# Optimization experiments

Hardware: AMD Instinct MI355X
Metric: run time of the kernel (lower is better)

The kernel has to match this reference:

```python
import jax, jax.numpy as jnp
import numpy as np
import math

D = 1024
N_HEAD = 16
HEAD_D = D // N_HEAD

def setup_inputs() -> dict:
    key = jax.random.key(0)
    ks = jax.random.split(key, 10)
    b, s = 4, 2048
    scale = 1.0 / math.sqrt(D)
    inp = {
        "decoder_hs": jax.random.normal(ks[0], (b, s, D), dtype=jnp.float32),
        "encoder_hs": jax.random.normal(ks[1], (b, s, D), dtype=jnp.float32),
        "Wq": jax.random.normal(ks[2], (D, D), dtype=jnp.float32) * scale,
        "bq": jnp.zeros((D,), dtype=jnp.float32),
        "Wk": jax.random.normal(ks[3], (D, D), dtype=jnp.float32) * scale,
        "bk": jnp.zeros((D,), dtype=jnp.float32),
        "Wv": jax.random.normal(ks[4], (D, D), dtype=jnp.float32) * scale,
        "bv": jnp.zeros((D,), dtype=jnp.float32),
        "Wp": jax.random.normal(ks[5], (D, D), dtype=jnp.float32) * scale,
        "bp": jnp.zeros((D,), dtype=jnp.float32),
    }
    return inp

def _split_heads(x, b, s):
    # [b, s, d] -> [b, n_head, s, head_d]
    return x.reshape(b, s, N_HEAD, HEAD_D).transpose(0, 2, 1, 3)

def reference(decoder_hs, encoder_hs, Wq, bq, Wk, bk, Wv, bv, Wp, bp):
    b, s, d = decoder_hs.shape
    # torch nn.Linear: y = x @ W.T + b
    q = _split_heads(decoder_hs @ Wq.T + bq, b, s)
    k = _split_heads(encoder_hs @ Wk.T + bk, b, s)
    v = _split_heads(encoder_hs @ Wv.T + bv, b, s)
    att = jnp.einsum('bhqd,bhkd->bhqk', q, k) * (1.0 / math.sqrt(HEAD_D))
    att = jax.nn.softmax(att, axis=-1)  # mask is None, dropout = 0 (eval)
    y = jnp.einsum('bhqk,bhkd->bhqd', att, v)
    y = y.transpose(0, 2, 1, 3).reshape(b, s, d)
    return y @ Wp.T + bp
```

## Files before the change

kernel.cpp:

```cpp
#include <hip/hip_runtime.h>
#include <hip/hip_bf16.h>

typedef __attribute__((ext_vector_type(8))) short bf16x8;
typedef __attribute__((ext_vector_type(4))) float floatx4;

#define MFMA_16x16x32(A, B, C) __builtin_amdgcn_mfma_f32_16x16x32_bf16(A, B, C, 0, 0, 0)

__device__ __forceinline__ unsigned short f2b(float f) {
    __hip_bfloat16 h = __float2bfloat16(f);
    unsigned short u;
    __builtin_memcpy(&u, &h, 2);
    return u;
}
__device__ __forceinline__ unsigned pk2(float a, float b) {
    __hip_bfloat162 h = __float22bfloat162_rn(float2{a, b});
    unsigned u;
    __builtin_memcpy(&u, &h, 4);
    return u;
}
__device__ __forceinline__ void async_lds16(const void* g, void* l) {
    __builtin_amdgcn_global_load_lds((__attribute__((address_space(1))) void*)g,
                                     (__attribute__((address_space(3))) void*)l, 16, 0, 0);
}

struct CvtArgs {
    const float* src[6];
    unsigned short* dst[6];
    float scale[6];
    int n8[6];
};
__global__ __launch_bounds__(256) void convert_kernel(CvtArgs a) {
    const int t = blockIdx.y;
    const int i = blockIdx.x * 256 + threadIdx.x;
    if (i >= a.n8[t]) return;
    const float sc = a.scale[t];
    const float4* s = (const float4*)a.src[t];
    const float4 x = s[2 * i], y = s[2 * i + 1];
    bf16x8 v;
    v[0] = (short)f2b(x.x * sc); v[1] = (short)f2b(x.y * sc);
    v[2] = (short)f2b(x.z * sc); v[3] = (short)f2b(x.w * sc);
    v[4] = (short)f2b(y.x * sc); v[5] = (short)f2b(y.y * sc);
    v[6] = (short)f2b(y.z * sc); v[7] = (short)f2b(y.w * sc);
    *(bf16x8*)(a.dst[t] + (size_t)i * 8) = v;
}

struct QKVArgs {
    const unsigned short* A[3];
    const unsigned short* B[3];
    const float* bias[3];
    float bscale[3];
    unsigned short* C[3];
};
__global__ __launch_bounds__(256) void gemm_qkv(QKVArgs args) {
    constexpr int M = 8192, N = 1024, K = 1024;
    __shared__ __align__(16) unsigned short As[2][4096];
    __shared__ __align__(16) unsigned short Bs[2][4096];

    const int z = blockIdx.z;
    const unsigned short* __restrict__ A = args.A[z];
    const unsigned short* __restrict__ B = args.B[z];
    const float* __restrict__ bias = args.bias[z];
    const float bsc = args.bscale[z];
    unsigned short* __restrict__ C = args.C[z];

    const int tid  = threadIdx.x;
    const int wave = tid >> 6;
    const int lane = tid & 63;
    const int l16  = lane & 15;
    const int quad = lane >> 4;
    const int bm = (blockIdx.x & 63) * 128;
    const int bn = (blockIdx.x >> 6) * 128;
    const int wm = (wave >> 1) * 64;
    const int wn = (wave & 1) * 64;

    const int srow = tid >> 2;
    const int skb  = (tid & 3) * 8;

    floatx4 acc[4][4] = {};

    auto stage = [&](int buf, int k0) {
        async_lds16(A + (size_t)(bm + srow) * K + skb + k0, &As[buf][tid * 8]);
        async_lds16(A + (size_t)(bm + 64 + srow) * K + skb + k0, &As[buf][2048 + tid * 8]);
        async_lds16(B + (size_t)(bn + srow) * K + skb + k0, &Bs[buf][tid * 8]);
        async_lds16(B + (size_t)(bn + 64 + srow) * K + skb + k0, &Bs[buf][2048 + tid * 8]);
    };

    stage(0, 0);
    for (int it = 0; it < K / 32; ++it) {
        __syncthreads();
        if (it + 1 < K / 32) stage((it + 1) & 1, (it + 1) * 32);
        const unsigned short* Ac = &As[it & 1][0];
        const unsigned short* Bc = &Bs[it & 1][0];

        bf16x8 af[4], bfr[4];
        #pragma unroll
        for (int i = 0; i < 4; ++i)
            af[i] = *(const bf16x8*)&Ac[(wm + i * 16 + l16) * 32 + quad * 8];
        #pragma unroll
        for (int j = 0; j < 4; ++j)
            bfr[j] = *(const bf16x8*)&Bc[(wn + j * 16 + l16) * 32 + quad * 8];
        #pragma unroll
        for (int i = 0; i < 4; ++i)
            #pragma unroll
            for (int j = 0; j < 4; ++j)
                acc[i][j] = MFMA_16x16x32(af[i], bfr[j], acc[i][j]);
    }

    if (z == 2) {
        __syncthreads();
        unsigned short* Tw = &As[0][0] + wave * (16 * 66);
        #pragma unroll
        for (int j = 0; j < 4; ++j) {
            const float bv = bias[bn + wn + j * 16 + l16] * bsc;
            #pragma unroll
            for (int i = 0; i < 4; ++i)
                #pragma unroll
                for (int r = 0; r < 4; ++r)
                    Tw[l16 * 66 + i * 16 + quad * 4 + r] = f2b(acc[i][j][r] + bv);
            __syncthreads();
            const int c2  = lane >> 2;
            const int tch = lane & 3;
            bf16x8 t0 = *(const bf16x8*)&Tw[c2 * 66 + tch * 16];
            bf16x8 t1 = *(const bf16x8*)&Tw[c2 * 66 + tch * 16 + 8];
            const size_t off = (size_t)(bn + wn + j * 16 + c2) * (size_t)M + (bm + wm + tch * 16);
            *(bf16x8*)&C[off]     = t0;
            *(bf16x8*)&C[off + 8] = t1;
            __syncthreads();
        }
    } else {
        #pragma unroll
        for (int i = 0; i < 4; ++i) {
            const int row = bm + wm + i * 16 + quad * 4;
            #pragma unroll
            for (int j = 0; j < 4; ++j) {
                const int col = bn + wn + j * 16 + l16;
                const float bv = bias[col] * bsc;
                #pragma unroll
                for (int r = 0; r < 4; ++r)
                    C[(size_t)(row + r) * N + col] = f2b(acc[i][j][r] + bv);
            }
        }
    }
}

__global__ __launch_bounds__(256) void gemm_out(
    const unsigned short* __restrict__ A, const unsigned short* __restrict__ B,
    const float* __restrict__ bias, float* __restrict__ C,
    int M, int N, int K)
{
    __shared__ __align__(16) unsigned short As[2][4096];
    __shared__ __align__(16) unsigned short Bs[2][4096];

    const int tid  = threadIdx.x;
    const int wave = tid >> 6;
    const int lane = tid & 63;
    const int l16  = lane & 15;
    const int quad = lane >> 4;
    const int bm = (blockIdx.x & 63) * 128;
    const int bn = (blockIdx.x >> 6) * 128;
    const int wm = (wave >> 1) * 64;
    const int wn = (wave & 1) * 64;

    const int srow = tid >> 2;
    const int skb  = (tid & 3) * 8;

    floatx4 acc[4][4] = {};

    auto stage = [&](int buf, int k0) {
        async_lds16(A + (size_t)(bm + srow) * K + skb + k0, &As[buf][tid * 8]);
        async_lds16(A + (size_t)(bm + 64 + srow) * K + skb + k0, &As[buf][2048 + tid * 8]);
        async_lds16(B + (size_t)(bn + srow) * K + skb + k0, &Bs[buf][tid * 8]);
        async_lds16(B + (size_t)(bn + 64 + srow) * K + skb + k0, &Bs[buf][2048 + tid * 8]);
    };

    stage(0, 0);
    for (int it = 0; it < K / 32; ++it) {
        __syncthreads();
        if (it + 1 < K / 32) stage((it + 1) & 1, (it + 1) * 32);
        const unsigned short* Ac = &As[it & 1][0];
        const unsigned short* Bc = &Bs[it & 1][0];

        bf16x8 af[4], bfr[4];
        #pragma unroll
        for (int i = 0; i < 4; ++i)
            af[i] = *(const bf16x8*)&Ac[(wm + i * 16 + l16) * 32 + quad * 8];
        #pragma unroll
        for (int j = 0; j < 4; ++j)
            bfr[j] = *(const bf16x8*)&Bc[(wn + j * 16 + l16) * 32 + quad * 8];
        #pragma unroll
        for (int i = 0; i < 4; ++i)
            #pragma unroll
            for (int j = 0; j < 4; ++j)
                acc[i][j] = MFMA_16x16x32(af[i], bfr[j], acc[i][j]);
    }

    #pragma unroll
    for (int i = 0; i < 4; ++i) {
        const int row = bm + wm + i * 16 + quad * 4;
        #pragma unroll
        for (int j = 0; j < 4; ++j) {
            const int col = bn + wn + j * 16 + l16;
            const float bv = bias[col];
            #pragma unroll
            for (int r = 0; r < 4; ++r)
                C[(size_t)(row + r) * N + col] = acc[i][j][r] + bv;
        }
    }
}

__global__ __launch_bounds__(512, 4) void attn_kernel(
    const unsigned short* __restrict__ Q, const unsigned short* __restrict__ Kg,
    const unsigned short* __restrict__ Vt, unsigned short* __restrict__ Y)
{
    __shared__ __align__(16) unsigned short Ks[2][4096];
    __shared__ __align__(16) unsigned short Vs[2][4096];
    __shared__ __align__(16) unsigned short Pt[8][32 * 68];

    const int tid  = threadIdx.x;
    const int wave = tid >> 6;
    const int lane = tid & 63;
    const int l16  = lane & 15;
    const int quad = lane >> 4;
    const int bh = blockIdx.x & 63;
    const int qt = blockIdx.x >> 6;
    const int b  = bh >> 4;
    const int h  = bh & 15;
    const int q0 = qt * 256 + wave * 32;
    const size_t base  = ((size_t)b * 2048) * 1024 + (size_t)h * 64;
    const size_t vbase = ((size_t)h * 64) * 8192 + (size_t)b * 2048;

    bf16x8 qf[2][2];
    #pragma unroll
    for (int nt = 0; nt < 2; ++nt) {
        const size_t qoff = base + (size_t)(q0 + nt * 16 + l16) * 1024 + quad * 8;
        qf[nt][0] = *(const bf16x8*)&Q[qoff];
        qf[nt][1] = *(const bf16x8*)&Q[qoff + 32];
    }

    bf16x8 ones;
    #pragma unroll
    for (int e = 0; e < 8; ++e) ones[e] = (short)0x3F80;
    const floatx4 ZERO4 = {0.f, 0.f, 0.f, 0.f};

    floatx4 o[2][4] = {};
    floatx4 rs[2] = {};

    const int rl_ = tid >> 3;
    const int cb  = tid & 7;
    const int csw = cb ^ (rl_ & 7);
    const int swz = l16 & 7;
    const int sw0 = (quad ^ swz) * 8;
    const int sw1 = ((4 + quad) ^ swz) * 8;
    const int krow = l16 * 64;
    const int prow = l16 * 68;
    const int pcol = quad * 4;

    unsigned short* Pw = &Pt[wave][0];

    auto stage = [&](int buf, int kv0) {
        async_lds16(&Kg[base + (size_t)(kv0 + rl_) * 1024 + csw * 8], &Ks[buf][tid * 8]);
        async_lds16(&Vt[vbase + (size_t)rl_ * 8192 + kv0 + csw * 8], &Vs[buf][tid * 8]);
    };

    stage(0, 0);
    for (int t = 0; t < 32; ++t) {
        __syncthreads();
        if (t < 31) stage((t + 1) & 1, (t + 1) * 64);
        const unsigned short* Kc = &Ks[t & 1][0];
        const unsigned short* Vc = &Vs[t & 1][0];

        floatx4 st[4][2];
        #pragma unroll
        for (int mt = 0; mt < 4; ++mt) {
            const bf16x8 kf0 = *(const bf16x8*)&Kc[mt * 1024 + krow + sw0];
            const bf16x8 kf1 = *(const bf16x8*)&Kc[mt * 1024 + krow + sw1];
            #pragma unroll
            for (int nt = 0; nt < 2; ++nt) {
                st[mt][nt] = MFMA_16x16x32(kf0, qf[nt][0], ZERO4);
                st[mt][nt] = MFMA_16x16x32(kf1, qf[nt][1], st[mt][nt]);
            }
        }

        #pragma unroll
        for (int mt = 0; mt < 4; ++mt) {
            #pragma unroll
            for (int nt = 0; nt < 2; ++nt) {
                uint2 w;
                w.x = pk2(__builtin_amdgcn_exp2f(st[mt][nt][0]),
                          __builtin_amdgcn_exp2f(st[mt][nt][1]));
                w.y = pk2(__builtin_amdgcn_exp2f(st[mt][nt][2]),
                          __builtin_amdgcn_exp2f(st[mt][nt][3]));
                *(uint2*)&Pw[nt * (16 * 68) + prow + mt * 16 + pcol] = w;
            }
        }

        #pragma unroll
        for (int kk = 0; kk < 2; ++kk) {
            const int swk = kk ? sw1 : sw0;
            bf16x8 pf[2];
            #pragma unroll
            for (int mq = 0; mq < 2; ++mq)
                pf[mq] = *(const bf16x8*)&Pw[mq * (16 * 68) + prow + kk * 32 + quad * 8];
            #pragma unroll
            for (int nd = 0; nd < 4; ++nd) {
                const bf16x8 vf = *(const bf16x8*)&Vc[nd * 1024 + krow + swk];
                #pragma unroll
                for (int mq = 0; mq < 2; ++mq)
                    o[mq][nd] = MFMA_16x16x32(pf[mq], vf, o[mq][nd]);
            }
            #pragma unroll
            for (int mq = 0; mq < 2; ++mq)
                rs[mq] = MFMA_16x16x32(pf[mq], ones, rs[mq]);
        }
    }

    #pragma unroll
    for (int mq = 0; mq < 2; ++mq) {
        #pragma unroll
        for (int r = 0; r < 4; ++r) {
            const float inv = 1.0f / rs[mq][r];
            const size_t row = q0 + mq * 16 + quad * 4 + r;
            #pragma unroll
            for (int nd = 0; nd < 4; ++nd)
                Y[base + row * 1024 + nd * 16 + l16] = f2b(o[mq][nd][r] * inv);
        }
    }
}

extern "C" void kernel_launch(void* const* d_in, const int* in_sizes, int n_in,
                              void* d_out, int out_size, void* d_ws, size_t ws_size,
                              hipStream_t stream)
{
    const float* dec = (const float*)d_in[0];
    const float* enc = (const float*)d_in[1];
    const float* Wq  = (const float*)d_in[2];
    const float* bq  = (const float*)d_in[3];
    const float* Wk  = (const float*)d_in[4];
    const float* bk  = (const float*)d_in[5];
    const float* Wv  = (const float*)d_in[6];
    const float* bv  = (const float*)d_in[7];
    const float* Wp  = (const float*)d_in[8];
    const float* bp  = (const float*)d_in[9];

    const size_t NTOK = 8192, DM = 1024;
    unsigned short* ws = (unsigned short*)d_ws;
    unsigned short* decB = ws;
    unsigned short* encB = decB + NTOK * DM;
    unsigned short* WqB  = encB + NTOK * DM;
    unsigned short* WkB  = WqB + DM * DM;
    unsigned short* WvB  = WkB + DM * DM;
    unsigned short* WpB  = WvB + DM * DM;
    unsigned short* Qb   = WpB + DM * DM;
    unsigned short* Kb   = Qb + NTOK * DM;
    unsigned short* VtG  = Kb + NTOK * DM;
    unsigned short* Yb   = VtG + NTOK * DM;

    const float C_SM = 0.18033688f;

    CvtArgs a;
    a.src[0] = dec; a.src[1] = enc; a.src[2] = Wq; a.src[3] = Wk; a.src[4] = Wv; a.src[5] = Wp;
    a.dst[0] = decB; a.dst[1] = encB; a.dst[2] = WqB; a.dst[3] = WkB; a.dst[4] = WvB; a.dst[5] = WpB;
    a.scale[0] = 1.f; a.scale[1] = 1.f; a.scale[2] = C_SM;
    a.scale[3] = 1.f; a.scale[4] = 1.f; a.scale[5] = 1.f;
    a.n8[0] = a.n8[1] = (int)(NTOK * DM / 8);
    a.n8[2] = a.n8[3] = a.n8[4] = a.n8[5] = (int)(DM * DM / 8);
    convert_kernel<<<dim3(4096, 6), 256, 0, stream>>>(a);

    QKVArgs qa;
    qa.A[0] = decB; qa.A[1] = encB; qa.A[2] = encB;
    qa.B[0] = WqB;  qa.B[1] = WkB;  qa.B[2] = WvB;
    qa.bias[0] = bq; qa.bias[1] = bk; qa.bias[2] = bv;
    qa.bscale[0] = C_SM; qa.bscale[1] = 1.f; qa.bscale[2] = 1.f;
    qa.C[0] = Qb;   qa.C[1] = Kb;   qa.C[2] = VtG;
    gemm_qkv<<<dim3(512, 1, 3), 256, 0, stream>>>(qa);

    attn_kernel<<<dim3(512), 512, 0, stream>>>(Qb, Kb, VtG, Yb);
    gemm_out<<<dim3(512), 256, 0, stream>>>(Yb, WpB, bp, (float*)d_out, 8192, 1024, 1024);
}
```

Measured before the change: 350.5 us.

## Software-pipeline QK^T of next tile with PV of current tile in attention

The attention loop is restructured so that each iteration computes the scores for KV tile t+1 while it accumulates P·V for tile t. The exp2 and P write for the next tile move after the PV MFMAs. The prologue now prefetches two tiles, and V gets a third LDS buffer so loads can run two tiles ahead. MFMA sections are wrapped in s_setprio to favour matrix issue across waves. The goal is to hide exp and LDS latency behind matrix work, at the cost of extra LDS and register pressure from holding the scores across the PV phase.

Measured after the change: 347.4 us. No clear change (-0.9%).

```diff
diff --git a/kernel.cpp b/kernel.cpp
--- a/kernel.cpp
+++ b/kernel.cpp
@@ -213,7 +213,7 @@
     const unsigned short* __restrict__ Vt, unsigned short* __restrict__ Y)
 {
     __shared__ __align__(16) unsigned short Ks[2][4096];
-    __shared__ __align__(16) unsigned short Vs[2][4096];
+    __shared__ __align__(16) unsigned short Vs[3][4096];
     __shared__ __align__(16) unsigned short Pt[8][32 * 68];
 
     const int tid  = threadIdx.x;
@@ -257,18 +257,18 @@
 
     unsigned short* Pw = &Pt[wave][0];
 
-    auto stage = [&](int buf, int kv0) {
+    auto stageK = [&](int buf, int kv0) {
         async_lds16(&Kg[base + (size_t)(kv0 + rl_) * 1024 + csw * 8], &Ks[buf][tid * 8]);
+    };
+    auto stageV = [&](int buf, int kv0) {
         async_lds16(&Vt[vbase + (size_t)rl_ * 8192 + kv0 + csw * 8], &Vs[buf][tid * 8]);
     };
 
-    stage(0, 0);
-    for (int t = 0; t < 32; ++t) {
-        __syncthreads();
-        if (t < 31) stage((t + 1) & 1, (t + 1) * 64);
-        const unsigned short* Kc = &Ks[t & 1][0];
-        const unsigned short* Vc = &Vs[t & 1][0];
-
+    stageK(0, 0);  stageV(0, 0);
+    stageK(1, 64); stageV(1, 64);
+    __syncthreads();
+    {
+        const unsigned short* Kc = &Ks[0][0];
         floatx4 st[4][2];
         #pragma unroll
         for (int mt = 0; mt < 4; ++mt) {
@@ -280,7 +280,6 @@
                 st[mt][nt] = MFMA_16x16x32(kf1, qf[nt][1], st[mt][nt]);
             }
         }
-
         #pragma unroll
         for (int mt = 0; mt < 4; ++mt) {
             #pragma unroll
@@ -293,25 +292,71 @@
                 *(uint2*)&Pw[nt * (16 * 68) + prow + mt * 16 + pcol] = w;
             }
         }
-
-        #pragma unroll
-        for (int kk = 0; kk < 2; ++kk) {
-            const int swk = kk ? sw1 : sw0;
-            bf16x8 pf[2];
-            #pragma unroll
-            for (int mq = 0; mq < 2; ++mq)
-                pf[mq] = *(const bf16x8*)&Pw[mq * (16 * 68) + prow + kk * 32 + quad * 8];
-            #pragma unroll
-            for (int nd = 0; nd < 4; ++nd) {
-                const bf16x8 vf = *(const bf16x8*)&Vc[nd * 1024 + krow + swk];
+    }
+
+    int vcur = 0;
+    int vstg = 2;
+
+    for (int t = 0; t < 32; ++t) {
+        __syncthreads();
+        if (t < 30) { stageK(t & 1, (t + 2) * 64); stageV(vstg, (t + 2) * 64); }
+
+        floatx4 st[4][2];
+        __builtin_amdgcn_s_setprio(1);
+        if (t < 31) {
+            const unsigned short* Kc = &Ks[(t + 1) & 1][0];
+            #pragma unroll
+            for (int mt = 0; mt < 4; ++mt) {
+                const bf16x8 kf0 = *(const bf16x8*)&Kc[mt * 1024 + krow + sw0];
+                const bf16x8 kf1 = *(const bf16x8*)&Kc[mt * 1024 + krow + sw1];
+                #pragma unroll
+                for (int nt = 0; nt < 2; ++nt) {
+                    st[mt][nt] = MFMA_16x16x32(kf0, qf[nt][0], ZERO4);
+                    st[mt][nt] = MFMA_16x16x32(kf1, qf[nt][1], st[mt][nt]);
+                }
+            }
+        }
+
+        {
+            const unsigned short* Vc = &Vs[vcur][0];
+            #pragma unroll
+            for (int kk = 0; kk < 2; ++kk) {
+                const int swk = kk ? sw1 : sw0;
+                bf16x8 pf[2];
                 #pragma unroll
                 for (int mq = 0; mq < 2; ++mq)
-                    o[mq][nd] = MFMA_16x16x32(pf[mq], vf, o[mq][nd]);
-            }
-            #pragma unroll
-            for (int mq = 0; mq < 2; ++mq)
-                rs[mq] = MFMA_16x16x32(pf[mq], ones, rs[mq]);
-        }
+                    pf[mq] = *(const bf16x8*)&Pw[mq * (16 * 68) + prow + kk * 32 + quad * 8];
+                #pragma unroll
+                for (int nd = 0; nd < 4; ++nd) {
+                    const bf16x8 vf = *(const bf16x8*)&Vc[nd * 1024 + krow + swk];
+                    #pragma unroll
+                    for (int mq = 0; mq < 2; ++mq)
+                        o[mq][nd] = MFMA_16x16x32(pf[mq], vf, o[mq][nd]);
+                }
+                #pragma unroll
+                for (int mq = 0; mq < 2; ++mq)
+                    rs[mq] = MFMA_16x16x32(pf[mq], ones, rs[mq]);
+            }
+        }
+        __builtin_amdgcn_s_setprio(0);
+
+        if (t < 31) {
+            #pragma unroll
+            for (int mt = 0; mt < 4; ++mt) {
+                #pragma unroll
+                for (int nt = 0; nt < 2; ++nt) {
+                    uint2 w;
+                    w.x = pk2(__builtin_amdgcn_exp2f(st[mt][nt][0]),
+                              __builtin_amdgcn_exp2f(st[mt][nt][1]));
+                    w.y = pk2(__builtin_amdgcn_exp2f(st[mt][nt][2]),
+                              __builtin_amdgcn_exp2f(st[mt][nt][3]));
+                    *(uint2*)&Pw[nt * (16 * 68) + prow + mt * 16 + pcol] = w;
+                }
+            }
+        }
+
+        vcur = (vcur == 2) ? 0 : vcur + 1;
+        vstg = (vstg == 2) ? 0 : vstg + 1;
     }
 
     #pragma unroll
```

## Rewrite attention with 32x32 MFMA and register-only P via permlane32 swap

Applied to the files above, without the earlier changes.

The attention kernel switches from 16x16x32 to 32x32x16 MFMAs. It computes S transposed so the exp'd P tile can be rearranged into A-operand layout with permlane32_swap instead of a round trip through LDS. Row sums are now accumulated with scalar adds instead of an MFMA against ones. The block shrinks to 4 waves (128 queries) with twice as many blocks, and s_setprio is raised around the MFMA bursts. This removes the per-tile LDS write/read of P and the extra row-sum MFMAs, but K/V tiles are now shared by fewer waves per block, which raises staging traffic relative to compute.

Result: faster. 324.8 us (-7.3%).

```diff
diff --git a/kernel.cpp b/kernel.cpp
--- a/kernel.cpp
+++ b/kernel.cpp
@@ -3,8 +3,11 @@
 
 typedef __attribute__((ext_vector_type(8))) short bf16x8;
 typedef __attribute__((ext_vector_type(4))) float floatx4;
+typedef __attribute__((ext_vector_type(16))) float floatx16;
+typedef __attribute__((ext_vector_type(2))) int int2v;
 
 #define MFMA_16x16x32(A, B, C) __builtin_amdgcn_mfma_f32_16x16x32_bf16(A, B, C, 0, 0, 0)
+#define MFMA_32x32x16(A, B, C) __builtin_amdgcn_mfma_f32_32x32x16_bf16(A, B, C, 0, 0, 0)
 
 __device__ __forceinline__ unsigned short f2b(float f) {
     __hip_bfloat16 h = __float2bfloat16(f);
@@ -17,6 +20,11 @@
     unsigned u;
     __builtin_memcpy(&u, &h, 4);
     return u;
+}
+__device__ __forceinline__ bf16x8 mk8(int a, int b, int c, int d) {
+    union { int u[4]; bf16x8 v; } x;
+    x.u[0] = a; x.u[1] = b; x.u[2] = c; x.u[3] = d;
+    return x.v;
 }
 __device__ __forceinline__ void async_lds16(const void* g, void* l) {
     __builtin_amdgcn_global_load_lds((__attribute__((address_space(1))) void*)g,
@@ -208,58 +216,77 @@
     }
 }
 
-__global__ __launch_bounds__(512, 4) void attn_kernel(
+__global__ __launch_bounds__(256, 4) void attn_kernel(
     const unsigned short* __restrict__ Q, const unsigned short* __restrict__ Kg,
     const unsigned short* __restrict__ Vt, unsigned short* __restrict__ Y)
 {
     __shared__ __align__(16) unsigned short Ks[2][4096];
     __shared__ __align__(16) unsigned short Vs[2][4096];
-    __shared__ __align__(16) unsigned short Pt[8][32 * 68];
+    __shared__ float rsb[4][32];
 
     const int tid  = threadIdx.x;
     const int wave = tid >> 6;
     const int lane = tid & 63;
-    const int l16  = lane & 15;
-    const int quad = lane >> 4;
+    const int l31  = lane & 31;
+    const int hi   = lane >> 5;
+    const int x7   = lane & 7;
     const int bh = blockIdx.x & 63;
     const int qt = blockIdx.x >> 6;
     const int b  = bh >> 4;
     const int h  = bh & 15;
-    const int q0 = qt * 256 + wave * 32;
+    const int q0 = qt * 128 + wave * 32;
     const size_t base  = ((size_t)b * 2048) * 1024 + (size_t)h * 64;
     const size_t vbase = ((size_t)h * 64) * 8192 + (size_t)b * 2048;
 
-    bf16x8 qf[2][2];
+    bf16x8 qf[4];
+    {
+        const size_t qrow = base + (size_t)(q0 + l31) * 1024 + hi * 8;
+        #pragma unroll
+        for (int ks = 0; ks < 4; ++ks)
+            qf[ks] = *(const bf16x8*)&Q[qrow + ks * 16];
+    }
+
+    const floatx16 Z16 = {0.f,0.f,0.f,0.f,0.f,0.f,0.f,0.f,
+                          0.f,0.f,0.f,0.f,0.f,0.f,0.f,0.f};
+
+    floatx16 o0 = Z16, o1 = Z16;
+    float racc = 0.f;
+
+    const int r0  = tid >> 3;
+    const int csw = (tid & 7) ^ (r0 & 7);
+
+    int co[4];
     #pragma unroll
-    for (int nt = 0; nt < 2; ++nt) {
-        const size_t qoff = base + (size_t)(q0 + nt * 16 + l16) * 1024 + quad * 8;
-        qf[nt][0] = *(const bf16x8*)&Q[qoff];
-        qf[nt][1] = *(const bf16x8*)&Q[qoff + 32];
-    }
-
-    bf16x8 ones;
-    #pragma unroll
-    for (int e = 0; e < 8; ++e) ones[e] = (short)0x3F80;
-    const floatx4 ZERO4 = {0.f, 0.f, 0.f, 0.f};
-
-    floatx4 o[2][4] = {};
-    floatx4 rs[2] = {};
-
-    const int rl_ = tid >> 3;
-    const int cb  = tid & 7;
-    const int csw = cb ^ (rl_ & 7);
-    const int swz = l16 & 7;
-    const int sw0 = (quad ^ swz) * 8;
-    const int sw1 = ((4 + quad) ^ swz) * 8;
-    const int krow = l16 * 64;
-    const int prow = l16 * 68;
-    const int pcol = quad * 4;
-
-    unsigned short* Pw = &Pt[wave][0];
+    for (int ks = 0; ks < 4; ++ks) co[ks] = (((ks * 2 + hi) ^ x7) * 8);
+    const int krow = l31 * 64;
 
     auto stage = [&](int buf, int kv0) {
-        async_lds16(&Kg[base + (size_t)(kv0 + rl_) * 1024 + csw * 8], &Ks[buf][tid * 8]);
-        async_lds16(&Vt[vbase + (size_t)rl_ * 8192 + kv0 + csw * 8], &Vs[buf][tid * 8]);
+        async_lds16(&Kg[base + (size_t)(kv0 + r0) * 1024 + csw * 8],      &Ks[buf][tid * 8]);
+        async_lds16(&Kg[base + (size_t)(kv0 + 32 + r0) * 1024 + csw * 8], &Ks[buf][2048 + tid * 8]);
+        async_lds16(&Vt[vbase + (size_t)r0 * 8192 + kv0 + csw * 8],        &Vs[buf][tid * 8]);
+        async_lds16(&Vt[vbase + (size_t)(r0 + 32) * 8192 + kv0 + csw * 8], &Vs[buf][2048 + tid * 8]);
+    };
+
+    auto procP = [&](const floatx16& st, bf16x8& paA, bf16x8& paB) {
+        float e[16];
+        #pragma unroll
+        for (int i = 0; i < 16; ++i) e[i] = __builtin_amdgcn_exp2f(st[i]);
+        racc += ((e[0]+e[1])+(e[2]+e[3])) + ((e[4]+e[5])+(e[6]+e[7]))
+              + ((e[8]+e[9])+(e[10]+e[11])) + ((e[12]+e[13])+(e[14]+e[15]));
+        const int w0 = (int)pk2(e[0],  e[1]);
+        const int w1 = (int)pk2(e[2],  e[3]);
+        const int w2 = (int)pk2(e[4],  e[5]);
+        const int w3 = (int)pk2(e[6],  e[7]);
+        const int w4 = (int)pk2(e[8],  e[9]);
+        const int w5 = (int)pk2(e[10], e[11]);
+        const int w6 = (int)pk2(e[12], e[13]);
+        const int w7 = (int)pk2(e[14], e[15]);
+        const int2v a0 = __builtin_amdgcn_permlane32_swap(w0, w2, false, false);
+        const int2v a1 = __builtin_amdgcn_permlane32_swap(w1, w3, false, false);
+        const int2v a2 = __builtin_amdgcn_permlane32_swap(w4, w6, false, false);
+        const int2v a3 = __builtin_amdgcn_permlane32_swap(w5, w7, false, false);
+        paA = mk8(a0.x, a1.x, a0.y, a1.y);
+        paB = mk8(a2.x, a3.x, a2.y, a3.y);
     };
 
     stage(0, 0);
@@ -269,60 +296,46 @@
         const unsigned short* Kc = &Ks[t & 1][0];
         const unsigned short* Vc = &Vs[t & 1][0];
 
-        floatx4 st[4][2];
-        #pragma unroll
-        for (int mt = 0; mt < 4; ++mt) {
-            const bf16x8 kf0 = *(const bf16x8*)&Kc[mt * 1024 + krow + sw0];
-            const bf16x8 kf1 = *(const bf16x8*)&Kc[mt * 1024 + krow + sw1];
-            #pragma unroll
-            for (int nt = 0; nt < 2; ++nt) {
-                st[mt][nt] = MFMA_16x16x32(kf0, qf[nt][0], ZERO4);
-                st[mt][nt] = MFMA_16x16x32(kf1, qf[nt][1], st[mt][nt]);
-            }
-        }
-
-        #pragma unroll
-        for (int mt = 0; mt < 4; ++mt) {
-            #pragma unroll
-            for (int nt = 0; nt < 2; ++nt) {
-                uint2 w;
-                w.x = pk2(__builtin_amdgcn_exp2f(st[mt][nt][0]),
-                          __builtin_amdgcn_exp2f(st[mt][nt][1]));
-                w.y = pk2(__builtin_amdgcn_exp2f(st[mt][nt][2]),
-                          __builtin_amdgcn_exp2f(st[mt][nt][3]));
-                *(uint2*)&Pw[nt * (16 * 68) + prow + mt * 16 + pcol] = w;
-            }
-        }
-
-        #pragma unroll
-        for (int kk = 0; kk < 2; ++kk) {
-            const int swk = kk ? sw1 : sw0;
-            bf16x8 pf[2];
-            #pragma unroll
-            for (int mq = 0; mq < 2; ++mq)
-                pf[mq] = *(const bf16x8*)&Pw[mq * (16 * 68) + prow + kk * 32 + quad * 8];
-            #pragma unroll
-            for (int nd = 0; nd < 4; ++nd) {
-                const bf16x8 vf = *(const bf16x8*)&Vc[nd * 1024 + krow + swk];
-                #pragma unroll
-                for (int mq = 0; mq < 2; ++mq)
-                    o[mq][nd] = MFMA_16x16x32(pf[mq], vf, o[mq][nd]);
-            }
-            #pragma unroll
-            for (int mq = 0; mq < 2; ++mq)
-                rs[mq] = MFMA_16x16x32(pf[mq], ones, rs[mq]);
-        }
-    }
-
+        floatx16 st0 = Z16, st1 = Z16;
+        __builtin_amdgcn_s_setprio(1);
+        #pragma unroll
+        for (int ks = 0; ks < 4; ++ks) {
+            const bf16x8 kf0 = *(const bf16x8*)&Kc[krow + co[ks]];
+            const bf16x8 kf1 = *(const bf16x8*)&Kc[2048 + krow + co[ks]];
+            st0 = MFMA_32x32x16(kf0, qf[ks], st0);
+            st1 = MFMA_32x32x16(kf1, qf[ks], st1);
+        }
+        __builtin_amdgcn_s_setprio(0);
+
+        bf16x8 pa[4];
+        procP(st0, pa[0], pa[1]);
+        procP(st1, pa[2], pa[3]);
+
+        __builtin_amdgcn_s_setprio(1);
+        #pragma unroll
+        for (int f = 0; f < 4; ++f) {
+            const bf16x8 v0 = *(const bf16x8*)&Vc[krow + co[f]];
+            const bf16x8 v1 = *(const bf16x8*)&Vc[2048 + krow + co[f]];
+            o0 = MFMA_32x32x16(pa[f], v0, o0);
+            o1 = MFMA_32x32x16(pa[f], v1, o1);
+        }
+        __builtin_amdgcn_s_setprio(0);
+    }
+
+    const int ri = __float_as_int(racc);
+    const int2v rsw = __builtin_amdgcn_permlane32_swap(ri, ri, false, false);
+    const float total = __int_as_float(rsw.x) + __int_as_float(rsw.y);
+    rsb[wave][l31] = total;
     #pragma unroll
-    for (int mq = 0; mq < 2; ++mq) {
-        #pragma unroll
-        for (int r = 0; r < 4; ++r) {
-            const float inv = 1.0f / rs[mq][r];
-            const size_t row = q0 + mq * 16 + quad * 4 + r;
-            #pragma unroll
-            for (int nd = 0; nd < 4; ++nd)
-                Y[base + row * 1024 + nd * 16 + l16] = f2b(o[mq][nd][r] * inv);
+    for (int g = 0; g < 4; ++g) {
+        const floatx4 rq = *(const floatx4*)&rsb[wave][4 * hi + 8 * g];
+        #pragma unroll
+        for (int e2 = 0; e2 < 4; ++e2) {
+            const float inv = 1.0f / rq[e2];
+            const int reg = g * 4 + e2;
+            const size_t row = q0 + 8 * g + 4 * hi + e2;
+            Y[base + row * 1024 + l31]      = f2b(o0[reg] * inv);
+            Y[base + row * 1024 + 32 + l31] = f2b(o1[reg] * inv);
         }
     }
 }
@@ -374,6 +387,6 @@
     qa.C[0] = Qb;   qa.C[1] = Kb;   qa.C[2] = VtG;
     gemm_qkv<<<dim3(512, 1, 3), 256, 0, stream>>>(qa);
 
-    attn_kernel<<<dim3(512), 512, 0, stream>>>(Qb, Kb, VtG, Yb);
+    attn_kernel<<<dim3(1024), 256, 0, stream>>>(Qb, Kb, VtG, Yb);
     gemm_out<<<dim3(512), 256, 0, stream>>>(Yb, WpB, bp, (float*)d_out, 8192, 1024, 1024);
 }
```
